# Performance work log

Hardware: AMD Instinct MI355X
Metric: run time of the kernel (lower is better)

Reference implementation:

```python
import jax, jax.numpy as jnp
import numpy as np

D_MODEL = 1024
N_HEADS = 16
N_KV = 4
HD = D_MODEL // N_HEADS  # 64
N_REP = N_HEADS // N_KV
WINDOW = 128
SCALE = HD ** -0.5
B, T = 2, 2048


def _rope(x):
    # x: [B, H, T, hd]; half-split rotate_half RoPE, base 10000
    t = x.shape[2]
    hd = x.shape[-1]
    inv_freq = 1.0 / (10000.0 ** (jnp.arange(0, hd, 2, dtype=jnp.float32) / hd))
    freqs = jnp.arange(t, dtype=jnp.float32)[:, None] * inv_freq[None, :]  # [T, hd/2]
    cos = jnp.cos(freqs)[None, None]  # [1,1,T,hd/2]
    sin = jnp.sin(freqs)[None, None]
    x1, x2 = x[..., : hd // 2], x[..., hd // 2:]
    return jnp.concatenate([x1 * cos - x2 * sin, x1 * sin + x2 * cos], axis=-1)


def setup_inputs() -> dict:
    key = jax.random.key(0)
    ks = jax.random.split(key, 6)
    s = 0.02
    return {
        "query": jax.random.normal(ks[0], (B, T, D_MODEL), dtype=jnp.float32),
        "Wq": jax.random.normal(ks[1], (D_MODEL, D_MODEL), dtype=jnp.float32) * s,
        "Wk": jax.random.normal(ks[2], (N_KV * HD, D_MODEL), dtype=jnp.float32) * s,
        "Wv": jax.random.normal(ks[3], (N_KV * HD, D_MODEL), dtype=jnp.float32) * s,
        "W1": jax.random.normal(ks[4], (4 * D_MODEL, D_MODEL), dtype=jnp.float32) * s,
        "W2": jax.random.normal(ks[5], (D_MODEL, 4 * D_MODEL), dtype=jnp.float32) * s,
    }


def reference(query, Wq, Wk, Wv, W1, W2):
    b, t, _ = query.shape
    # QKV projections (nn.Linear, no bias): x @ W.T
    q = (query @ Wq.T).reshape(b, t, N_HEADS, HD).transpose(0, 2, 1, 3)  # [B,H,T,hd]
    k = (query @ Wk.T).reshape(b, t, N_KV, HD).transpose(0, 2, 1, 3)    # [B,Hkv,T,hd]
    v = (query @ Wv.T).reshape(b, t, N_KV, HD).transpose(0, 2, 1, 3)
    # Rotary embeddings on q/k (self-attention)
    q = _rope(q)
    k = _rope(k)
    # GQA: repeat kv heads (kv-head-major ordering, matches torch expand+reshape)
    k = jnp.repeat(k, N_REP, axis=1)
    v = jnp.repeat(v, N_REP, axis=1)
    # scores + causal sliding-window band mask (True = masked)
    scores = jnp.einsum("bhqd,bhkd->bhqk", q, k) * SCALE
    i = jnp.arange(t)[:, None]
    j = jnp.arange(t)[None, :]
    mask = (j > i) | (j < i - (WINDOW - 1))  # causal window of size WINDOW
    scores = jnp.where(mask[None, None], jnp.float32(-1e30), scores)
    attn = jax.nn.softmax(scores, axis=-1)
    out = jnp.einsum("bhqk,bhkd->bhqd", attn, v)
    out = out.transpose(0, 2, 1, 3).reshape(b, t, D_MODEL)
    # out_proj: Linear(d,4d) -> SiLU -> Linear(4d,d)
    h = out @ W1.T
    h = h * jax.nn.sigmoid(h)
    return h @ W2.T
```

## Files before the change

kernel.cpp:

```cpp
#include <hip/hip_runtime.h>
#include <math.h>


typedef __bf16 bf16x8 __attribute__((ext_vector_type(8)));
typedef __bf16 bf16x4 __attribute__((ext_vector_type(4)));
typedef float  f32x4  __attribute__((ext_vector_type(4)));

extern __shared__ __align__(16) char smem[];

#define GLOAD_LDS16(g, l) __builtin_amdgcn_global_load_lds(               \
    (const __attribute__((address_space(1))) void*)(g),                   \
    (__attribute__((address_space(3))) void*)(l), 16, 0, 0)

__device__ __forceinline__ unsigned pk2(float a, float b) {
    union { __bf16 h[2]; unsigned u; } t;
    t.h[0] = (__bf16)a; t.h[1] = (__bf16)b;
    return t.u;
}

__device__ __forceinline__ int xcd_swz(int bid, int n) {
    return (bid & 7) * (n >> 3) + (bid >> 3);
}

__global__ __launch_bounds__(256) void MultiAttention_60722247631706_conv(
    const float* x, const float* Wq, const float* Wk, const float* Wv,
    const float* W1, const float* W2, float* out, float* ws, int phase)
{
    __bf16* xbf    = (__bf16*)(ws + 6291456);
    __bf16* wqkvbf = (__bf16*)(ws + 8388608);
    __bf16* w1bf   = (__bf16*)(ws + 10485760);
    __bf16* w2bf   = (__bf16*)(ws + 8388608);
    const int tid = threadIdx.x;

    if (phase == 5) {
        const long long total4 = 9961472 / 4;
        for (long long i4 = (long long)blockIdx.x * 256 + tid; i4 < total4;
             i4 += (long long)gridDim.x * 256) {
            const long long i = i4 * 4;
            const float* src; __bf16* dst;
            if (i < 4194304)      { src = x  + i;             dst = xbf    + i; }
            else if (i < 5242880) { src = Wq + (i - 4194304); dst = wqkvbf + (i - 4194304); }
            else if (i < 5505024) { src = Wk + (i - 5242880); dst = wqkvbf + (i - 4194304); }
            else if (i < 5767168) { src = Wv + (i - 5505024); dst = wqkvbf + (i - 4194304); }
            else                  { src = W1 + (i - 5767168); dst = w1bf   + (i - 5767168); }
            const f32x4 v = *(const f32x4*)src;
            bf16x4 o;
            o[0] = (__bf16)v[0]; o[1] = (__bf16)v[1];
            o[2] = (__bf16)v[2]; o[3] = (__bf16)v[3];
            *(bf16x4*)dst = o;
        }
    } else {
        const long long total4 = 4194304 / 4;
        for (long long i4 = (long long)blockIdx.x * 256 + tid; i4 < total4;
             i4 += (long long)gridDim.x * 256) {
            const long long i = i4 * 4;
            const f32x4 v = *(const f32x4*)(W2 + i);
            bf16x4 o;
            o[0] = (__bf16)v[0]; o[1] = (__bf16)v[1];
            o[2] = (__bf16)v[2]; o[3] = (__bf16)v[3];
            *(bf16x4*)(w2bf + i) = o;
        }
        const f32x4 z = {0.f, 0.f, 0.f, 0.f};
        for (long long i4 = (long long)blockIdx.x * 256 + tid; i4 < total4;
             i4 += (long long)gridDim.x * 256) {
            *(f32x4*)(out + i4 * 4) = z;
        }
    }
}

__global__ __launch_bounds__(256, 4) void MultiAttention_60722247631706_attn(
    float* ws)
{
    const __bf16* qbf  = (const __bf16*)ws;
    const __bf16* kbf  = (const __bf16*)(ws + 2097152);
    const __bf16* vtbf = (const __bf16*)(ws + 2621440);
    __bf16*       obf  = (__bf16*)(ws + 8388608);

    const int sb  = xcd_swz(blockIdx.x, 1024);
    const int qt  = sb & 127;
    const int kvh = (sb >> 7) & 3;
    const int b   = sb >> 9;
    const int q0  = qt * 16;
    const int wb  = q0 - 128;

    const int tid  = threadIdx.x;
    const int w    = tid >> 6;
    const int lane = tid & 63;
    const int l16  = lane & 15;
    const int quad = lane >> 4;
    const int h    = kvh * 4 + w;

    const __bf16* Kb = kbf + (size_t)b * 2048 * 256 + kvh * 64;
    const __bf16* Vb = vtbf + (size_t)(b * 4 + kvh) * 64 * 2048;

    bf16x8 qf[2];
#pragma unroll
    for (int kk = 0; kk < 2; ++kk)
        qf[kk] = *(const bf16x8*)(qbf + (size_t)(b * 2048 + q0 + l16) * 1024
                                  + h * 64 + kk * 32 + quad * 8);

    f32x4 oacc[4];
#pragma unroll
    for (int dn = 0; dn < 4; ++dn) {
        f32x4 z = {0.f, 0.f, 0.f, 0.f};
        oacc[dn] = z;
    }
    float m_run = -1e30f, l_run = 0.f;
    const int kclip = -wb;

    for (int kb = 0; kb < 3; ++kb) {
        f32x4 s[4];
#pragma unroll
        for (int km = 0; km < 4; ++km) {
            f32x4 z = {0.f, 0.f, 0.f, 0.f};
            s[km] = z;
        }
#pragma unroll
        for (int kk = 0; kk < 2; ++kk) {
            bf16x8 kf[4];
#pragma unroll
            for (int km = 0; km < 4; ++km) {
                int row = wb + kb * 64 + km * 16 + l16;
                row = (row >= 0 && row < 2048) ? row : 0;
                kf[km] = *(const bf16x8*)(Kb + (size_t)row * 256
                                          + kk * 32 + quad * 8);
            }
#pragma unroll
            for (int km = 0; km < 4; ++km)
                s[km] = __builtin_amdgcn_mfma_f32_16x16x32_bf16(
                    kf[km], qf[kk], s[km], 0, 0, 0);
        }

        float mx = -1e30f;
#pragma unroll
        for (int km = 0; km < 4; ++km)
#pragma unroll
            for (int r = 0; r < 4; ++r) {
                const int kl  = kb * 64 + km * 16 + quad * 4 + r;
                const int dlt = kl - l16;
                const bool ok = (dlt >= 1) && (dlt <= 128) && (kl >= kclip);
                const float sv = ok ? s[km][r] : -1e30f;
                s[km][r] = sv;
                mx = fmaxf(mx, sv);
            }
        mx = fmaxf(mx, __shfl_xor(mx, 16));
        mx = fmaxf(mx, __shfl_xor(mx, 32));
        const float mnew = fmaxf(fmaxf(m_run, mx), -1e20f);
        const float corr = expf(m_run - mnew);
        m_run = mnew;
        float rowsum = 0.f;
        unsigned cu[4][2];
#pragma unroll
        for (int km = 0; km < 4; ++km) {
#pragma unroll
            for (int r = 0; r < 4; ++r) {
                const float p = expf(s[km][r] - mnew);
                s[km][r] = p;
                rowsum += p;
            }
            cu[km][0] = pk2(s[km][0], s[km][1]);
            cu[km][1] = pk2(s[km][2], s[km][3]);
        }
        rowsum += __shfl_xor(rowsum, 16);
        rowsum += __shfl_xor(rowsum, 32);
        l_run = l_run * corr + rowsum;

#pragma unroll
        for (int r = 0; r < 4; ++r) {
            const float f = __shfl(corr, (lane & 48) | (quad * 4 + r));
            oacc[0][r] *= f; oacc[1][r] *= f;
            oacc[2][r] *= f; oacc[3][r] *= f;
        }

#pragma unroll
        for (int kk = 0; kk < 2; ++kk) {
            bf16x8 vf[4];
#pragma unroll
            for (int dn = 0; dn < 4; ++dn) {
                int t = wb + kb * 64 + kk * 32 + quad * 8;
                t = (t >= 0 && t <= 2040) ? t : 0;
                vf[dn] = *(const bf16x8*)(Vb + (size_t)(dn * 16 + l16) * 2048 + t);
            }
            const int srcA = ((quad & 1) * 32) + l16;
            const int hi   = quad >> 1;
            const unsigned a0 = (unsigned)__shfl((int)cu[2*kk  ][0], srcA);
            const unsigned a1 = (unsigned)__shfl((int)cu[2*kk  ][1], srcA);
            const unsigned b0 = (unsigned)__shfl((int)cu[2*kk+1][0], srcA);
            const unsigned b1 = (unsigned)__shfl((int)cu[2*kk+1][1], srcA);
            const unsigned c0 = (unsigned)__shfl((int)cu[2*kk  ][0], srcA + 16);
            const unsigned c1 = (unsigned)__shfl((int)cu[2*kk  ][1], srcA + 16);
            const unsigned d0 = (unsigned)__shfl((int)cu[2*kk+1][0], srcA + 16);
            const unsigned d1 = (unsigned)__shfl((int)cu[2*kk+1][1], srcA + 16);
            union { unsigned u[4]; bf16x8 v; } af;
            af.u[0] = hi ? b0 : a0;
            af.u[1] = hi ? b1 : a1;
            af.u[2] = hi ? d0 : c0;
            af.u[3] = hi ? d1 : c1;
#pragma unroll
            for (int dn = 0; dn < 4; ++dn)
                oacc[dn] = __builtin_amdgcn_mfma_f32_16x16x32_bf16(
                    af.v, vf[dn], oacc[dn], 0, 0, 0);
        }
    }

    const float rl = 1.f / l_run;
#pragma unroll
    for (int r = 0; r < 4; ++r) {
        const float f = __shfl(rl, (lane & 48) | (quad * 4 + r));
        const int q = q0 + quad * 4 + r;
        __bf16* op = obf + ((size_t)(b * 2048 + q)) * 1024 + h * 64 + l16;
#pragma unroll
        for (int dn = 0; dn < 4; ++dn)
            op[dn * 16] = (__bf16)(oacc[dn][r] * f);
    }
}

__global__ __launch_bounds__(256, 4) void MultiAttention_60722247631706_p0(
    float* ws)
{
    __bf16* qbf    = (__bf16*)ws;
    __bf16* kbf    = (__bf16*)(ws + 2097152);
    __bf16* vtbf   = (__bf16*)(ws + 2621440);
    __bf16* xbf    = (__bf16*)(ws + 6291456);
    __bf16* wqkvbf = (__bf16*)(ws + 8388608);

    const int tid = threadIdx.x;

    __bf16* As = (__bf16*)smem;
    __bf16* Bs = As + 64 * 64;

    const int bid  = xcd_swz(blockIdx.x, 768);
    const int tm   = bid / 12;
    const int tn   = bid % 12;
    const int w    = tid >> 6;
    const int lane = tid & 63;
    const int wr   = w >> 1;
    const int wc   = w & 1;
    const int l16  = lane & 15;
    const int quad = lane >> 4;
    const int srow = lane >> 3;
    const int sch  = ((lane & 7) ^ srow) * 8;

    const __bf16* ga0 = xbf    + (size_t)(tm * 64  + w * 16 + srow) * 1024 + sch;
    const __bf16* gb0 = wqkvbf + (size_t)(tn * 128 + w * 32 + srow) * 1024 + sch;

    f32x4 zero = {0.f, 0.f, 0.f, 0.f};
    f32x4 acc[2][4];
#pragma unroll
    for (int mi = 0; mi < 2; ++mi)
#pragma unroll
        for (int ni = 0; ni < 4; ++ni) acc[mi][ni] = zero;

    for (int k0 = 0; k0 < 1024; k0 += 64) {
#pragma unroll
        for (int i = 0; i < 2; ++i)
            GLOAD_LDS16(ga0 + (size_t)i * 8 * 1024 + k0, As + (w * 16 + i * 8) * 64);
#pragma unroll
        for (int i = 0; i < 4; ++i)
            GLOAD_LDS16(gb0 + (size_t)i * 8 * 1024 + k0, Bs + (w * 32 + i * 8) * 64);
        __syncthreads();
#pragma unroll
        for (int kk = 0; kk < 2; ++kk) {
            const int cs = ((kk * 4 + quad) ^ (l16 & 7)) * 8;
            bf16x8 af[2], bfr[4];
#pragma unroll
            for (int mi = 0; mi < 2; ++mi)
                af[mi] = *(const bf16x8*)(As + (size_t)(wr * 32 + mi * 16 + l16) * 64 + cs);
#pragma unroll
            for (int ni = 0; ni < 4; ++ni)
                bfr[ni] = *(const bf16x8*)(Bs + (size_t)(wc * 64 + ni * 16 + l16) * 64 + cs);
#pragma unroll
            for (int mi = 0; mi < 2; ++mi)
#pragma unroll
                for (int ni = 0; ni < 4; ++ni)
                    acc[mi][ni] = __builtin_amdgcn_mfma_f32_16x16x32_bf16(
                        af[mi], bfr[ni], acc[mi][ni], 0, 0, 0);
        }
        __syncthreads();
    }

    const int mbase = tm * 64 + wr * 32;
    const int nbase = tn * 128 + wc * 64;

    if (nbase < 1280) {
        const bool isQ = nbase < 1024;
        const float inv1 = powf(10000.f, -(float)l16 / 32.f);
        const float inv2 = powf(10000.f, -(float)(16 + l16) / 32.f);
#pragma unroll
        for (int mi = 0; mi < 2; ++mi) {
#pragma unroll
            for (int r = 0; r < 4; ++r) {
                const int m = mbase + mi * 16 + quad * 4 + r;
                const int t = m & 2047;
                float v0 = acc[mi][0][r], v1 = acc[mi][1][r];
                float v2 = acc[mi][2][r], v3 = acc[mi][3][r];
                const float a1 = (float)t * inv1, a2 = (float)t * inv2;
                const float c1 = cosf(a1), s1 = sinf(a1);
                const float c2 = cosf(a2), s2 = sinf(a2);
                float n0 = v0 * c1 - v2 * s1;
                float n2 = v0 * s1 + v2 * c1;
                float n1 = v1 * c2 - v3 * s2;
                float n3 = v1 * s2 + v3 * c2;
                if (isQ) { n0 *= 0.125f; n1 *= 0.125f; n2 *= 0.125f; n3 *= 0.125f; }
                __bf16* dst = isQ
                    ? qbf + (size_t)m * 1024 + nbase + l16
                    : kbf + (size_t)m * 256 + (nbase - 1024) + l16;
                dst[0]  = (__bf16)n0; dst[16] = (__bf16)n1;
                dst[32] = (__bf16)n2; dst[48] = (__bf16)n3;
            }
        }
    } else {
        const int kvh = (nbase - 1280) >> 6;
        const int bb  = mbase >> 11;
        const int tb  = mbase & 2047;
#pragma unroll
        for (int mi = 0; mi < 2; ++mi) {
#pragma unroll
            for (int ni = 0; ni < 4; ++ni) {
                const int d = ni * 16 + l16;
                bf16x4 pv;
                pv[0] = (__bf16)acc[mi][ni][0]; pv[1] = (__bf16)acc[mi][ni][1];
                pv[2] = (__bf16)acc[mi][ni][2]; pv[3] = (__bf16)acc[mi][ni][3];
                *(bf16x4*)(vtbf + ((size_t)(bb * 4 + kvh) * 64 + d) * 2048
                           + tb + mi * 16 + quad * 4) = pv;
            }
        }
    }
}

__global__ __launch_bounds__(256, 4) void MultiAttention_60722247631706_ffn1(
    float* ws)
{
    __bf16* obf  = (__bf16*)(ws + 8388608);
    __bf16* w1bf = (__bf16*)(ws + 10485760);
    __bf16* hbf  = (__bf16*)ws;

    const int tid = threadIdx.x;

    __bf16* As = (__bf16*)smem;
    __bf16* Bs = As + 128 * 64;

    const int bid  = xcd_swz(blockIdx.x, 1024);
    const int tm   = bid >> 5;
    const int tn   = bid & 31;
    const int w    = tid >> 6;
    const int lane = tid & 63;
    const int wr   = w >> 1;
    const int wc   = w & 1;
    const int l16  = lane & 15;
    const int quad = lane >> 4;
    const int srow = lane >> 3;
    const int sch  = ((lane & 7) ^ srow) * 8;

    const __bf16* ga0 = obf  + (size_t)(tm * 128 + w * 32 + srow) * 1024 + sch;
    const __bf16* gb0 = w1bf + (size_t)(tn * 128 + w * 32 + srow) * 1024 + sch;

    f32x4 zero = {0.f, 0.f, 0.f, 0.f};
    f32x4 acc[4][4];
#pragma unroll
    for (int mi = 0; mi < 4; ++mi)
#pragma unroll
        for (int ni = 0; ni < 4; ++ni) acc[mi][ni] = zero;

    for (int k0 = 0; k0 < 1024; k0 += 64) {
#pragma unroll
        for (int i = 0; i < 4; ++i) {
            GLOAD_LDS16(ga0 + (size_t)i * 8 * 1024 + k0, As + (w * 32 + i * 8) * 64);
            GLOAD_LDS16(gb0 + (size_t)i * 8 * 1024 + k0, Bs + (w * 32 + i * 8) * 64);
        }
        __syncthreads();
#pragma unroll
        for (int kk = 0; kk < 2; ++kk) {
            const int cs = ((kk * 4 + quad) ^ (l16 & 7)) * 8;
            bf16x8 af[4], bfr[4];
#pragma unroll
            for (int mi = 0; mi < 4; ++mi)
                af[mi] = *(const bf16x8*)(As + (size_t)(wr * 64 + mi * 16 + l16) * 64 + cs);
#pragma unroll
            for (int ni = 0; ni < 4; ++ni)
                bfr[ni] = *(const bf16x8*)(Bs + (size_t)(wc * 64 + ni * 16 + l16) * 64 + cs);
#pragma unroll
            for (int mi = 0; mi < 4; ++mi)
#pragma unroll
                for (int ni = 0; ni < 4; ++ni)
                    acc[mi][ni] = __builtin_amdgcn_mfma_f32_16x16x32_bf16(
                        af[mi], bfr[ni], acc[mi][ni], 0, 0, 0);
        }
        __syncthreads();
    }

#pragma unroll
    for (int mi = 0; mi < 4; ++mi) {
#pragma unroll
        for (int r = 0; r < 4; ++r) {
            const int m = tm * 128 + wr * 64 + mi * 16 + quad * 4 + r;
            __bf16* hp = hbf + (size_t)m * 4096 + tn * 128 + wc * 64 + l16;
#pragma unroll
            for (int ni = 0; ni < 4; ++ni) {
                const float v = acc[mi][ni][r];
                hp[ni * 16] = (__bf16)(v / (1.f + expf(-v)));
            }
        }
    }
}

__global__ __launch_bounds__(256, 4) void MultiAttention_60722247631706_ffn2(
    float* out, float* ws)
{
    __bf16* hbf  = (__bf16*)ws;
    __bf16* w2bf = (__bf16*)(ws + 8388608);

    int bid = xcd_swz(blockIdx.x, 1024);
    const int ks = bid >> 9;  bid &= 511;
    const int tm = bid >> 3;
    const int tn = bid & 7;
    const int kbase = ks * 2048;

    const int tid  = threadIdx.x;
    const int w    = tid >> 6;
    const int lane = tid & 63;
    const int wr   = w >> 1;
    const int wc   = w & 1;
    const int l16  = lane & 15;
    const int quad = lane >> 4;
    const int srow = lane >> 3;
    const int sch  = ((lane & 7) ^ srow) * 8;

    __bf16* As = (__bf16*)smem;
    __bf16* Bs = As + 64 * 64;

    const __bf16* ga0 = hbf  + (size_t)(tm * 64  + w * 16 + srow) * 4096 + kbase + sch;
    const __bf16* gb0 = w2bf + (size_t)(tn * 128 + w * 32 + srow) * 4096 + kbase + sch;

    f32x4 zero = {0.f, 0.f, 0.f, 0.f};
    f32x4 acc[2][4];
#pragma unroll
    for (int mi = 0; mi < 2; ++mi)
#pragma unroll
        for (int ni = 0; ni < 4; ++ni) acc[mi][ni] = zero;

    for (int k0 = 0; k0 < 2048; k0 += 64) {
#pragma unroll
        for (int i = 0; i < 2; ++i)
            GLOAD_LDS16(ga0 + (size_t)i * 8 * 4096 + k0, As + (w * 16 + i * 8) * 64);
#pragma unroll
        for (int i = 0; i < 4; ++i)
            GLOAD_LDS16(gb0 + (size_t)i * 8 * 4096 + k0, Bs + (w * 32 + i * 8) * 64);
        __syncthreads();
#pragma unroll
        for (int kk = 0; kk < 2; ++kk) {
            const int cs = ((kk * 4 + quad) ^ (l16 & 7)) * 8;
            bf16x8 af[2], bfr[4];
#pragma unroll
            for (int mi = 0; mi < 2; ++mi)
                af[mi] = *(const bf16x8*)(As + (size_t)(wr * 32 + mi * 16 + l16) * 64 + cs);
#pragma unroll
            for (int ni = 0; ni < 4; ++ni)
                bfr[ni] = *(const bf16x8*)(Bs + (size_t)(wc * 64 + ni * 16 + l16) * 64 + cs);
#pragma unroll
            for (int mi = 0; mi < 2; ++mi)
#pragma unroll
                for (int ni = 0; ni < 4; ++ni)
                    acc[mi][ni] = __builtin_amdgcn_mfma_f32_16x16x32_bf16(
                        af[mi], bfr[ni], acc[mi][ni], 0, 0, 0);
        }
        __syncthreads();
    }

#pragma unroll
    for (int mi = 0; mi < 2; ++mi) {
#pragma unroll
        for (int r = 0; r < 4; ++r) {
            const int m = tm * 64 + wr * 32 + mi * 16 + quad * 4 + r;
            float* op = out + (size_t)m * 1024 + tn * 128 + wc * 64 + l16;
#pragma unroll
            for (int ni = 0; ni < 4; ++ni)
                atomicAdd(op + ni * 16, acc[mi][ni][r]);
        }
    }
}

extern "C" void kernel_launch(void* const* d_in, const int* in_sizes, int n_in,
                              void* d_out, int out_size, void* d_ws, size_t ws_size,
                              hipStream_t stream)
{
    const float* x  = (const float*)d_in[0];
    const float* Wq = (const float*)d_in[1];
    const float* Wk = (const float*)d_in[2];
    const float* Wv = (const float*)d_in[3];
    const float* W1 = (const float*)d_in[4];
    const float* W2 = (const float*)d_in[5];
    float* out = (float*)d_out;
    float* ws  = (float*)d_ws;

    const int P0_LDS   = (64 + 128) * 64 * 2;
    const int FFN1_LDS = 2 * 128 * 64 * 2;
    const int FFN2_LDS = (64 + 128) * 64 * 2;

    MultiAttention_60722247631706_conv<<<2048, 256, 0, stream>>>(
        x, Wq, Wk, Wv, W1, W2, out, ws, 5);
    MultiAttention_60722247631706_p0<<<768, 256, P0_LDS, stream>>>(ws);
    MultiAttention_60722247631706_attn<<<1024, 256, 0, stream>>>(ws);
    MultiAttention_60722247631706_ffn1<<<1024, 256, FFN1_LDS, stream>>>(ws);
    MultiAttention_60722247631706_conv<<<1024, 256, 0, stream>>>(
        x, Wq, Wk, Wv, W1, W2, out, ws, 6);
    MultiAttention_60722247631706_ffn2<<<1024, 256, FFN2_LDS, stream>>>(out, ws);
}
```

Baseline: 247.0 us.

## Pre-tile bf16 operands into MFMA fragment order and drop LDS staging in GEMMs

The conversion kernels now write x, Wqkv, W1 and W2 in a 16x32 fragment-tiled layout. The attention and FFN1 epilogues write their outputs in that same tiled layout. The three GEMMs then load MFMA operands straight from global memory as contiguous 16-byte vectors, with no LDS staging and no __syncthreads. FFN2 also moves to a 128x128 tile with 512 blocks. This removes LDS traffic and barriers, but every wave now reloads the same operands from L2 with no shared reuse inside a block, and global latency is not hidden by any prefetch.

Measured after the change: 344.5 us. 1.39x slower.

```diff
diff --git a/kernel.cpp b/kernel.cpp
--- a/kernel.cpp
+++ b/kernel.cpp
@@ -5,12 +5,6 @@
 typedef __bf16 bf16x8 __attribute__((ext_vector_type(8)));
 typedef __bf16 bf16x4 __attribute__((ext_vector_type(4)));
 typedef float  f32x4  __attribute__((ext_vector_type(4)));
-
-extern __shared__ __align__(16) char smem[];
-
-#define GLOAD_LDS16(g, l) __builtin_amdgcn_global_load_lds(               \
-    (const __attribute__((address_space(1))) void*)(g),                   \
-    (__attribute__((address_space(3))) void*)(l), 16, 0, 0)
 
 __device__ __forceinline__ unsigned pk2(float a, float b) {
     union { __bf16 h[2]; unsigned u; } t;
@@ -22,49 +16,72 @@
     return (bid & 7) * (n >> 3) + (bid >> 3);
 }
 
-__global__ __launch_bounds__(256) void MultiAttention_60722247631706_conv(
+__device__ __forceinline__ void fm_chunk(const float* src, __bf16* dst8) {
+    const f32x4 a = *(const f32x4*)src;
+    const f32x4 b = *(const f32x4*)(src + 4);
+    bf16x8 o;
+    o[0] = (__bf16)a[0]; o[1] = (__bf16)a[1];
+    o[2] = (__bf16)a[2]; o[3] = (__bf16)a[3];
+    o[4] = (__bf16)b[0]; o[5] = (__bf16)b[1];
+    o[6] = (__bf16)b[2]; o[7] = (__bf16)b[3];
+    *(bf16x8*)dst8 = o;
+}
+
+__global__ __launch_bounds__(256) void MultiAttention_60722247631706_conv5(
     const float* x, const float* Wq, const float* Wk, const float* Wv,
-    const float* W1, const float* W2, float* out, float* ws, int phase)
-{
-    __bf16* xbf    = (__bf16*)(ws + 6291456);
-    __bf16* wqkvbf = (__bf16*)(ws + 8388608);
-    __bf16* w1bf   = (__bf16*)(ws + 10485760);
-    __bf16* w2bf   = (__bf16*)(ws + 8388608);
+    const float* W1, float* out, float* ws)
+{
+    __bf16* xt    = (__bf16*)(ws + 6291456);
+    __bf16* wqkvt = (__bf16*)(ws + 8388608);
+    __bf16* w1t   = (__bf16*)(ws + 10485760);
     const int tid = threadIdx.x;
 
-    if (phase == 5) {
-        const long long total4 = 9961472 / 4;
-        for (long long i4 = (long long)blockIdx.x * 256 + tid; i4 < total4;
-             i4 += (long long)gridDim.x * 256) {
-            const long long i = i4 * 4;
-            const float* src; __bf16* dst;
-            if (i < 4194304)      { src = x  + i;             dst = xbf    + i; }
-            else if (i < 5242880) { src = Wq + (i - 4194304); dst = wqkvbf + (i - 4194304); }
-            else if (i < 5505024) { src = Wk + (i - 5242880); dst = wqkvbf + (i - 4194304); }
-            else if (i < 5767168) { src = Wv + (i - 5505024); dst = wqkvbf + (i - 4194304); }
-            else                  { src = W1 + (i - 5767168); dst = w1bf   + (i - 5767168); }
-            const f32x4 v = *(const f32x4*)src;
-            bf16x4 o;
-            o[0] = (__bf16)v[0]; o[1] = (__bf16)v[1];
-            o[2] = (__bf16)v[2]; o[3] = (__bf16)v[3];
-            *(bf16x4*)dst = o;
-        }
-    } else {
-        const long long total4 = 4194304 / 4;
-        for (long long i4 = (long long)blockIdx.x * 256 + tid; i4 < total4;
-             i4 += (long long)gridDim.x * 256) {
-            const long long i = i4 * 4;
-            const f32x4 v = *(const f32x4*)(W2 + i);
-            bf16x4 o;
-            o[0] = (__bf16)v[0]; o[1] = (__bf16)v[1];
-            o[2] = (__bf16)v[2]; o[3] = (__bf16)v[3];
-            *(bf16x4*)(w2bf + i) = o;
-        }
-        const f32x4 z = {0.f, 0.f, 0.f, 0.f};
-        for (long long i4 = (long long)blockIdx.x * 256 + tid; i4 < total4;
-             i4 += (long long)gridDim.x * 256) {
-            *(f32x4*)(out + i4 * 4) = z;
-        }
+    const int XC = 524288, WQC = 196608, W1C = 524288;
+    const int total = XC + WQC + W1C;
+    for (int i = blockIdx.x * 256 + tid; i < total;
+         i += gridDim.x * 256) {
+        int c; const float* srcm; __bf16* dstm; int ldsrc = 1024;
+        int rowoff = 0;
+        if (i < XC)            { c = i;            srcm = x;  dstm = xt; }
+        else if (i < XC + WQC) { c = i - XC;       srcm = 0;  dstm = wqkvt; }
+        else                   { c = i - XC - WQC; srcm = W1; dstm = w1t; }
+        const int kq  = c & 3;
+        const int nin = (c >> 2) & 15;
+        const int kt  = (c >> 6) & 31;
+        const int nt  = c >> 11;
+        const int row = nt * 16 + nin;
+        const int col = kt * 32 + kq * 8;
+        const float* src;
+        if (srcm) {
+            src = srcm + (size_t)row * ldsrc + col;
+        } else {
+            if (row < 1024)      src = Wq + (size_t)row * 1024 + col;
+            else if (row < 1280) src = Wk + (size_t)(row - 1024) * 1024 + col;
+            else                 src = Wv + (size_t)(row - 1280) * 1024 + col;
+        }
+        fm_chunk(src, dstm + (size_t)c * 8);
+        (void)rowoff;
+    }
+    const f32x4 z = {0.f, 0.f, 0.f, 0.f};
+    for (int i4 = blockIdx.x * 256 + tid; i4 < 1048576;
+         i4 += gridDim.x * 256) {
+        *(f32x4*)(out + (size_t)i4 * 4) = z;
+    }
+}
+
+__global__ __launch_bounds__(256) void MultiAttention_60722247631706_conv6(
+    const float* W2, float* ws)
+{
+    __bf16* w2t = (__bf16*)(ws + 8388608);
+    const int tid = threadIdx.x;
+    for (int c = blockIdx.x * 256 + tid; c < 524288;
+         c += gridDim.x * 256) {
+        const int kq  = c & 3;
+        const int nin = (c >> 2) & 15;
+        const int kt  = (c >> 6) & 127;
+        const int nt  = c >> 13;
+        const float* src = W2 + (size_t)(nt * 16 + nin) * 4096 + kt * 32 + kq * 8;
+        fm_chunk(src, w2t + (size_t)c * 8);
     }
 }
 
@@ -204,14 +221,14 @@
     }
 
     const float rl = 1.f / l_run;
+    __bf16* ob = obf + ((size_t)(b * 128 + qt) * 32 + h * 2) * 512 + l16;
 #pragma unroll
     for (int r = 0; r < 4; ++r) {
         const float f = __shfl(rl, (lane & 48) | (quad * 4 + r));
-        const int q = q0 + quad * 4 + r;
-        __bf16* op = obf + ((size_t)(b * 2048 + q)) * 1024 + h * 64 + l16;
+        __bf16* obr = ob + (quad * 4 + r) * 32;
 #pragma unroll
         for (int dn = 0; dn < 4; ++dn)
-            op[dn * 16] = (__bf16)(oacc[dn][r] * f);
+            obr[(dn >> 1) * 512 + (dn & 1) * 16] = (__bf16)(oacc[dn][r] * f);
     }
 }
 
@@ -221,14 +238,10 @@
     __bf16* qbf    = (__bf16*)ws;
     __bf16* kbf    = (__bf16*)(ws + 2097152);
     __bf16* vtbf   = (__bf16*)(ws + 2621440);
-    __bf16* xbf    = (__bf16*)(ws + 6291456);
-    __bf16* wqkvbf = (__bf16*)(ws + 8388608);
-
-    const int tid = threadIdx.x;
-
-    __bf16* As = (__bf16*)smem;
-    __bf16* Bs = As + 64 * 64;
-
+    const __bf16* xt    = (const __bf16*)(ws + 6291456);
+    const __bf16* wqkvt = (const __bf16*)(ws + 8388608);
+
+    const int tid  = threadIdx.x;
     const int bid  = xcd_swz(blockIdx.x, 768);
     const int tm   = bid / 12;
     const int tn   = bid % 12;
@@ -238,11 +251,7 @@
     const int wc   = w & 1;
     const int l16  = lane & 15;
     const int quad = lane >> 4;
-    const int srow = lane >> 3;
-    const int sch  = ((lane & 7) ^ srow) * 8;
-
-    const __bf16* ga0 = xbf    + (size_t)(tm * 64  + w * 16 + srow) * 1024 + sch;
-    const __bf16* gb0 = wqkvbf + (size_t)(tn * 128 + w * 32 + srow) * 1024 + sch;
+    const int lo   = l16 * 32 + quad * 8;
 
     f32x4 zero = {0.f, 0.f, 0.f, 0.f};
     f32x4 acc[2][4];
@@ -253,22 +262,17 @@
 
     for (int k0 = 0; k0 < 1024; k0 += 64) {
 #pragma unroll
-        for (int i = 0; i < 2; ++i)
-            GLOAD_LDS16(ga0 + (size_t)i * 8 * 1024 + k0, As + (w * 16 + i * 8) * 64);
-#pragma unroll
-        for (int i = 0; i < 4; ++i)
-            GLOAD_LDS16(gb0 + (size_t)i * 8 * 1024 + k0, Bs + (w * 32 + i * 8) * 64);
-        __syncthreads();
-#pragma unroll
         for (int kk = 0; kk < 2; ++kk) {
-            const int cs = ((kk * 4 + quad) ^ (l16 & 7)) * 8;
+            const int kt = (k0 >> 5) + kk;
             bf16x8 af[2], bfr[4];
 #pragma unroll
             for (int mi = 0; mi < 2; ++mi)
-                af[mi] = *(const bf16x8*)(As + (size_t)(wr * 32 + mi * 16 + l16) * 64 + cs);
+                af[mi] = *(const bf16x8*)(xt +
+                    ((size_t)(tm * 4 + wr * 2 + mi) * 32 + kt) * 512 + lo);
 #pragma unroll
             for (int ni = 0; ni < 4; ++ni)
-                bfr[ni] = *(const bf16x8*)(Bs + (size_t)(wc * 64 + ni * 16 + l16) * 64 + cs);
+                bfr[ni] = *(const bf16x8*)(wqkvt +
+                    ((size_t)(tn * 8 + wc * 4 + ni) * 32 + kt) * 512 + lo);
 #pragma unroll
             for (int mi = 0; mi < 2; ++mi)
 #pragma unroll
@@ -276,7 +280,6 @@
                     acc[mi][ni] = __builtin_amdgcn_mfma_f32_16x16x32_bf16(
                         af[mi], bfr[ni], acc[mi][ni], 0, 0, 0);
         }
-        __syncthreads();
     }
 
     const int mbase = tm * 64 + wr * 32;
@@ -331,15 +334,11 @@
 __global__ __launch_bounds__(256, 4) void MultiAttention_60722247631706_ffn1(
     float* ws)
 {
-    __bf16* obf  = (__bf16*)(ws + 8388608);
-    __bf16* w1bf = (__bf16*)(ws + 10485760);
-    __bf16* hbf  = (__bf16*)ws;
-
-    const int tid = threadIdx.x;
-
-    __bf16* As = (__bf16*)smem;
-    __bf16* Bs = As + 128 * 64;
-
+    const __bf16* ot  = (const __bf16*)(ws + 8388608);
+    const __bf16* w1t = (const __bf16*)(ws + 10485760);
+    __bf16*       ht  = (__bf16*)ws;
+
+    const int tid  = threadIdx.x;
     const int bid  = xcd_swz(blockIdx.x, 1024);
     const int tm   = bid >> 5;
     const int tn   = bid & 31;
@@ -349,11 +348,7 @@
     const int wc   = w & 1;
     const int l16  = lane & 15;
     const int quad = lane >> 4;
-    const int srow = lane >> 3;
-    const int sch  = ((lane & 7) ^ srow) * 8;
-
-    const __bf16* ga0 = obf  + (size_t)(tm * 128 + w * 32 + srow) * 1024 + sch;
-    const __bf16* gb0 = w1bf + (size_t)(tn * 128 + w * 32 + srow) * 1024 + sch;
+    const int lo   = l16 * 32 + quad * 8;
 
     f32x4 zero = {0.f, 0.f, 0.f, 0.f};
     f32x4 acc[4][4];
@@ -364,21 +359,17 @@
 
     for (int k0 = 0; k0 < 1024; k0 += 64) {
 #pragma unroll
-        for (int i = 0; i < 4; ++i) {
-            GLOAD_LDS16(ga0 + (size_t)i * 8 * 1024 + k0, As + (w * 32 + i * 8) * 64);
-            GLOAD_LDS16(gb0 + (size_t)i * 8 * 1024 + k0, Bs + (w * 32 + i * 8) * 64);
-        }
-        __syncthreads();
-#pragma unroll
         for (int kk = 0; kk < 2; ++kk) {
-            const int cs = ((kk * 4 + quad) ^ (l16 & 7)) * 8;
+            const int kt = (k0 >> 5) + kk;
             bf16x8 af[4], bfr[4];
 #pragma unroll
             for (int mi = 0; mi < 4; ++mi)
-                af[mi] = *(const bf16x8*)(As + (size_t)(wr * 64 + mi * 16 + l16) * 64 + cs);
+                af[mi] = *(const bf16x8*)(ot +
+                    ((size_t)(tm * 8 + wr * 4 + mi) * 32 + kt) * 512 + lo);
 #pragma unroll
             for (int ni = 0; ni < 4; ++ni)
-                bfr[ni] = *(const bf16x8*)(Bs + (size_t)(wc * 64 + ni * 16 + l16) * 64 + cs);
+                bfr[ni] = *(const bf16x8*)(w1t +
+                    ((size_t)(tn * 8 + wc * 4 + ni) * 32 + kt) * 512 + lo);
 #pragma unroll
             for (int mi = 0; mi < 4; ++mi)
 #pragma unroll
@@ -386,19 +377,20 @@
                     acc[mi][ni] = __builtin_amdgcn_mfma_f32_16x16x32_bf16(
                         af[mi], bfr[ni], acc[mi][ni], 0, 0, 0);
         }
-        __syncthreads();
     }
 
 #pragma unroll
     for (int mi = 0; mi < 4; ++mi) {
+        const int mtile = tm * 8 + wr * 4 + mi;
+        __bf16* hb = ht + ((size_t)mtile * 128 + (tn * 4 + wc * 2)) * 512 + l16;
 #pragma unroll
         for (int r = 0; r < 4; ++r) {
-            const int m = tm * 128 + wr * 64 + mi * 16 + quad * 4 + r;
-            __bf16* hp = hbf + (size_t)m * 4096 + tn * 128 + wc * 64 + l16;
+            __bf16* hr = hb + (quad * 4 + r) * 32;
 #pragma unroll
             for (int ni = 0; ni < 4; ++ni) {
                 const float v = acc[mi][ni][r];
-                hp[ni * 16] = (__bf16)(v / (1.f + expf(-v)));
+                hr[(ni >> 1) * 512 + (ni & 1) * 16] =
+                    (__bf16)(v / (1.f + expf(-v)));
             }
         }
     }
@@ -407,14 +399,14 @@
 __global__ __launch_bounds__(256, 4) void MultiAttention_60722247631706_ffn2(
     float* out, float* ws)
 {
-    __bf16* hbf  = (__bf16*)ws;
-    __bf16* w2bf = (__bf16*)(ws + 8388608);
-
-    int bid = xcd_swz(blockIdx.x, 1024);
-    const int ks = bid >> 9;  bid &= 511;
+    const __bf16* ht  = (const __bf16*)ws;
+    const __bf16* w2t = (const __bf16*)(ws + 8388608);
+
+    int bid = xcd_swz(blockIdx.x, 512);
+    const int ks = bid >> 8;  bid &= 255;
     const int tm = bid >> 3;
     const int tn = bid & 7;
-    const int kbase = ks * 2048;
+    const int ktb = ks * 64;
 
     const int tid  = threadIdx.x;
     const int w    = tid >> 6;
@@ -423,55 +415,42 @@
     const int wc   = w & 1;
     const int l16  = lane & 15;
     const int quad = lane >> 4;
-    const int srow = lane >> 3;
-    const int sch  = ((lane & 7) ^ srow) * 8;
-
-    __bf16* As = (__bf16*)smem;
-    __bf16* Bs = As + 64 * 64;
-
-    const __bf16* ga0 = hbf  + (size_t)(tm * 64  + w * 16 + srow) * 4096 + kbase + sch;
-    const __bf16* gb0 = w2bf + (size_t)(tn * 128 + w * 32 + srow) * 4096 + kbase + sch;
+    const int lo   = l16 * 32 + quad * 8;
 
     f32x4 zero = {0.f, 0.f, 0.f, 0.f};
-    f32x4 acc[2][4];
-#pragma unroll
-    for (int mi = 0; mi < 2; ++mi)
+    f32x4 acc[4][4];
+#pragma unroll
+    for (int mi = 0; mi < 4; ++mi)
 #pragma unroll
         for (int ni = 0; ni < 4; ++ni) acc[mi][ni] = zero;
 
     for (int k0 = 0; k0 < 2048; k0 += 64) {
 #pragma unroll
-        for (int i = 0; i < 2; ++i)
-            GLOAD_LDS16(ga0 + (size_t)i * 8 * 4096 + k0, As + (w * 16 + i * 8) * 64);
-#pragma unroll
-        for (int i = 0; i < 4; ++i)
-            GLOAD_LDS16(gb0 + (size_t)i * 8 * 4096 + k0, Bs + (w * 32 + i * 8) * 64);
-        __syncthreads();
-#pragma unroll
         for (int kk = 0; kk < 2; ++kk) {
-            const int cs = ((kk * 4 + quad) ^ (l16 & 7)) * 8;
-            bf16x8 af[2], bfr[4];
-#pragma unroll
-            for (int mi = 0; mi < 2; ++mi)
-                af[mi] = *(const bf16x8*)(As + (size_t)(wr * 32 + mi * 16 + l16) * 64 + cs);
+            const int kt = ktb + (k0 >> 5) + kk;
+            bf16x8 af[4], bfr[4];
+#pragma unroll
+            for (int mi = 0; mi < 4; ++mi)
+                af[mi] = *(const bf16x8*)(ht +
+                    ((size_t)(tm * 8 + wr * 4 + mi) * 128 + kt) * 512 + lo);
 #pragma unroll
             for (int ni = 0; ni < 4; ++ni)
-                bfr[ni] = *(const bf16x8*)(Bs + (size_t)(wc * 64 + ni * 16 + l16) * 64 + cs);
-#pragma unroll
-            for (int mi = 0; mi < 2; ++mi)
+                bfr[ni] = *(const bf16x8*)(w2t +
+                    ((size_t)(tn * 8 + wc * 4 + ni) * 128 + kt) * 512 + lo);
+#pragma unroll
+            for (int mi = 0; mi < 4; ++mi)
 #pragma unroll
                 for (int ni = 0; ni < 4; ++ni)
                     acc[mi][ni] = __builtin_amdgcn_mfma_f32_16x16x32_bf16(
                         af[mi], bfr[ni], acc[mi][ni], 0, 0, 0);
         }
-        __syncthreads();
-    }
-
-#pragma unroll
-    for (int mi = 0; mi < 2; ++mi) {
+    }
+
+#pragma unroll
+    for (int mi = 0; mi < 4; ++mi) {
 #pragma unroll
         for (int r = 0; r < 4; ++r) {
-            const int m = tm * 64 + wr * 32 + mi * 16 + quad * 4 + r;
+            const int m = tm * 128 + wr * 64 + mi * 16 + quad * 4 + r;
             float* op = out + (size_t)m * 1024 + tn * 128 + wc * 64 + l16;
 #pragma unroll
             for (int ni = 0; ni < 4; ++ni)
@@ -493,16 +472,11 @@
     float* out = (float*)d_out;
     float* ws  = (float*)d_ws;
 
-    const int P0_LDS   = (64 + 128) * 64 * 2;
-    const int FFN1_LDS = 2 * 128 * 64 * 2;
-    const int FFN2_LDS = (64 + 128) * 64 * 2;
-
-    MultiAttention_60722247631706_conv<<<2048, 256, 0, stream>>>(
-        x, Wq, Wk, Wv, W1, W2, out, ws, 5);
-    MultiAttention_60722247631706_p0<<<768, 256, P0_LDS, stream>>>(ws);
+    MultiAttention_60722247631706_conv5<<<2048, 256, 0, stream>>>(
+        x, Wq, Wk, Wv, W1, out, ws);
+    MultiAttention_60722247631706_p0<<<768, 256, 0, stream>>>(ws);
     MultiAttention_60722247631706_attn<<<1024, 256, 0, stream>>>(ws);
-    MultiAttention_60722247631706_ffn1<<<1024, 256, FFN1_LDS, stream>>>(ws);
-    MultiAttention_60722247631706_conv<<<1024, 256, 0, stream>>>(
-        x, Wq, Wk, Wv, W1, W2, out, ws, 6);
-    MultiAttention_60722247631706_ffn2<<<1024, 256, FFN2_LDS, stream>>>(out, ws);
-}
+    MultiAttention_60722247631706_ffn1<<<1024, 256, 0, stream>>>(ws);
+    MultiAttention_60722247631706_conv6<<<1024, 256, 0, stream>>>(W2, ws);
+    MultiAttention_60722247631706_ffn2<<<512, 256, 0, stream>>>(out, ws);
+}
```

## Pre-swizzle FFN weights into MFMA fragment order and load B directly from global

Applied to the files above, without the earlier changes.

The fp32-to-bf16 conversion of W1 and W2 now writes them in a tiled layout that matches the MFMA B-fragment order. The FFN GEMMs can then read B operands straight from global memory into registers, with no LDS staging. This shrinks LDS use per block and removes LDS traffic and bank conflicts for B. The cost is that B-operand reuse across waves now depends on L1/L2 caching instead of shared memory, and global-load latency is exposed inside the k-loop. The zeroing of the output is also moved into the first conversion kernel.

Measured after the change: 282.9 us. +14.5%, slower.

```diff
diff --git a/kernel.cpp b/kernel.cpp
--- a/kernel.cpp
+++ b/kernel.cpp
@@ -22,49 +22,66 @@
     return (bid & 7) * (n >> 3) + (bid >> 3);
 }
 
-__global__ __launch_bounds__(256) void MultiAttention_60722247631706_conv(
+__device__ __forceinline__ void fm_chunk(const float* src, __bf16* dst8) {
+    const f32x4 a = *(const f32x4*)src;
+    const f32x4 b = *(const f32x4*)(src + 4);
+    bf16x8 o;
+    o[0] = (__bf16)a[0]; o[1] = (__bf16)a[1];
+    o[2] = (__bf16)a[2]; o[3] = (__bf16)a[3];
+    o[4] = (__bf16)b[0]; o[5] = (__bf16)b[1];
+    o[6] = (__bf16)b[2]; o[7] = (__bf16)b[3];
+    *(bf16x8*)dst8 = o;
+}
+
+__global__ __launch_bounds__(256) void MultiAttention_60722247631706_conv5(
     const float* x, const float* Wq, const float* Wk, const float* Wv,
-    const float* W1, const float* W2, float* out, float* ws, int phase)
+    const float* W1, float* out, float* ws)
 {
     __bf16* xbf    = (__bf16*)(ws + 6291456);
     __bf16* wqkvbf = (__bf16*)(ws + 8388608);
-    __bf16* w1bf   = (__bf16*)(ws + 10485760);
-    __bf16* w2bf   = (__bf16*)(ws + 8388608);
+    __bf16* w1t    = (__bf16*)(ws + 10485760);
     const int tid = threadIdx.x;
 
-    if (phase == 5) {
-        const long long total4 = 9961472 / 4;
-        for (long long i4 = (long long)blockIdx.x * 256 + tid; i4 < total4;
-             i4 += (long long)gridDim.x * 256) {
-            const long long i = i4 * 4;
-            const float* src; __bf16* dst;
-            if (i < 4194304)      { src = x  + i;             dst = xbf    + i; }
-            else if (i < 5242880) { src = Wq + (i - 4194304); dst = wqkvbf + (i - 4194304); }
-            else if (i < 5505024) { src = Wk + (i - 5242880); dst = wqkvbf + (i - 4194304); }
-            else if (i < 5767168) { src = Wv + (i - 5505024); dst = wqkvbf + (i - 4194304); }
-            else                  { src = W1 + (i - 5767168); dst = w1bf   + (i - 5767168); }
-            const f32x4 v = *(const f32x4*)src;
-            bf16x4 o;
-            o[0] = (__bf16)v[0]; o[1] = (__bf16)v[1];
-            o[2] = (__bf16)v[2]; o[3] = (__bf16)v[3];
-            *(bf16x4*)dst = o;
-        }
-    } else {
-        const long long total4 = 4194304 / 4;
-        for (long long i4 = (long long)blockIdx.x * 256 + tid; i4 < total4;
-             i4 += (long long)gridDim.x * 256) {
-            const long long i = i4 * 4;
-            const f32x4 v = *(const f32x4*)(W2 + i);
-            bf16x4 o;
-            o[0] = (__bf16)v[0]; o[1] = (__bf16)v[1];
-            o[2] = (__bf16)v[2]; o[3] = (__bf16)v[3];
-            *(bf16x4*)(w2bf + i) = o;
-        }
-        const f32x4 z = {0.f, 0.f, 0.f, 0.f};
-        for (long long i4 = (long long)blockIdx.x * 256 + tid; i4 < total4;
-             i4 += (long long)gridDim.x * 256) {
-            *(f32x4*)(out + i4 * 4) = z;
-        }
+    const long long total4 = 5767168 / 4;
+    for (long long i4 = (long long)blockIdx.x * 256 + tid; i4 < total4;
+         i4 += (long long)gridDim.x * 256) {
+        const long long i = i4 * 4;
+        const float* src; __bf16* dst;
+        if (i < 4194304)      { src = x  + i;             dst = xbf    + i; }
+        else if (i < 5242880) { src = Wq + (i - 4194304); dst = wqkvbf + (i - 4194304); }
+        else if (i < 5505024) { src = Wk + (i - 5242880); dst = wqkvbf + (i - 4194304); }
+        else                  { src = Wv + (i - 5505024); dst = wqkvbf + (i - 4194304); }
+        const f32x4 v = *(const f32x4*)src;
+        bf16x4 o;
+        o[0] = (__bf16)v[0]; o[1] = (__bf16)v[1];
+        o[2] = (__bf16)v[2]; o[3] = (__bf16)v[3];
+        *(bf16x4*)dst = o;
+    }
+    for (int c = blockIdx.x * 256 + tid; c < 524288; c += gridDim.x * 256) {
+        const int kq  = c & 3;
+        const int nin = (c >> 2) & 15;
+        const int kt  = (c >> 6) & 31;
+        const int nt  = c >> 11;
+        const float* src = W1 + (size_t)(nt * 16 + nin) * 1024 + kt * 32 + kq * 8;
+        fm_chunk(src, w1t + (size_t)c * 8);
+    }
+    const f32x4 z = {0.f, 0.f, 0.f, 0.f};
+    for (int i4 = blockIdx.x * 256 + tid; i4 < 1048576; i4 += gridDim.x * 256)
+        *(f32x4*)(out + (size_t)i4 * 4) = z;
+}
+
+__global__ __launch_bounds__(256) void MultiAttention_60722247631706_conv6(
+    const float* W2, float* ws)
+{
+    __bf16* w2t = (__bf16*)(ws + 8388608);
+    const int tid = threadIdx.x;
+    for (int c = blockIdx.x * 256 + tid; c < 524288; c += gridDim.x * 256) {
+        const int kq  = c & 3;
+        const int nin = (c >> 2) & 15;
+        const int kt  = (c >> 6) & 127;
+        const int nt  = c >> 13;
+        const float* src = W2 + (size_t)(nt * 16 + nin) * 4096 + kt * 32 + kq * 8;
+        fm_chunk(src, w2t + (size_t)c * 8);
     }
 }
 
@@ -331,14 +348,13 @@
 __global__ __launch_bounds__(256, 4) void MultiAttention_60722247631706_ffn1(
     float* ws)
 {
-    __bf16* obf  = (__bf16*)(ws + 8388608);
-    __bf16* w1bf = (__bf16*)(ws + 10485760);
-    __bf16* hbf  = (__bf16*)ws;
+    __bf16*       obf = (__bf16*)(ws + 8388608);
+    const __bf16* w1t = (const __bf16*)(ws + 10485760);
+    __bf16*       hbf = (__bf16*)ws;
 
     const int tid = threadIdx.x;
 
     __bf16* As = (__bf16*)smem;
-    __bf16* Bs = As + 128 * 64;
 
     const int bid  = xcd_swz(blockIdx.x, 1024);
     const int tm   = bid >> 5;
@@ -351,9 +367,10 @@
     const int quad = lane >> 4;
     const int srow = lane >> 3;
     const int sch  = ((lane & 7) ^ srow) * 8;
-
-    const __bf16* ga0 = obf  + (size_t)(tm * 128 + w * 32 + srow) * 1024 + sch;
-    const __bf16* gb0 = w1bf + (size_t)(tn * 128 + w * 32 + srow) * 1024 + sch;
+    const int lo   = l16 * 32 + quad * 8;
+
+    const __bf16* ga0 = obf + (size_t)(tm * 128 + w * 32 + srow) * 1024 + sch;
+    const __bf16* wb0 = w1t + (size_t)(tn * 8 + wc * 4) * 32 * 512 + lo;
 
     f32x4 zero = {0.f, 0.f, 0.f, 0.f};
     f32x4 acc[4][4];
@@ -364,21 +381,21 @@
 
     for (int k0 = 0; k0 < 1024; k0 += 64) {
 #pragma unroll
-        for (int i = 0; i < 4; ++i) {
+        for (int i = 0; i < 4; ++i)
             GLOAD_LDS16(ga0 + (size_t)i * 8 * 1024 + k0, As + (w * 32 + i * 8) * 64);
-            GLOAD_LDS16(gb0 + (size_t)i * 8 * 1024 + k0, Bs + (w * 32 + i * 8) * 64);
-        }
         __syncthreads();
 #pragma unroll
         for (int kk = 0; kk < 2; ++kk) {
+            const int kt = (k0 >> 5) + kk;
+            bf16x8 bfr[4];
+#pragma unroll
+            for (int ni = 0; ni < 4; ++ni)
+                bfr[ni] = *(const bf16x8*)(wb0 + ((size_t)ni * 32 + kt) * 512);
             const int cs = ((kk * 4 + quad) ^ (l16 & 7)) * 8;
-            bf16x8 af[4], bfr[4];
+            bf16x8 af[4];
 #pragma unroll
             for (int mi = 0; mi < 4; ++mi)
                 af[mi] = *(const bf16x8*)(As + (size_t)(wr * 64 + mi * 16 + l16) * 64 + cs);
-#pragma unroll
-            for (int ni = 0; ni < 4; ++ni)
-                bfr[ni] = *(const bf16x8*)(Bs + (size_t)(wc * 64 + ni * 16 + l16) * 64 + cs);
 #pragma unroll
             for (int mi = 0; mi < 4; ++mi)
 #pragma unroll
@@ -407,14 +424,15 @@
 __global__ __launch_bounds__(256, 4) void MultiAttention_60722247631706_ffn2(
     float* out, float* ws)
 {
-    __bf16* hbf  = (__bf16*)ws;
-    __bf16* w2bf = (__bf16*)(ws + 8388608);
+    const __bf16* hbf = (const __bf16*)ws;
+    const __bf16* w2t = (const __bf16*)(ws + 8388608);
 
     int bid = xcd_swz(blockIdx.x, 1024);
     const int ks = bid >> 9;  bid &= 511;
     const int tm = bid >> 3;
     const int tn = bid & 7;
     const int kbase = ks * 2048;
+    const int ktb   = ks * 64;
 
     const int tid  = threadIdx.x;
     const int w    = tid >> 6;
@@ -425,12 +443,12 @@
     const int quad = lane >> 4;
     const int srow = lane >> 3;
     const int sch  = ((lane & 7) ^ srow) * 8;
+    const int lo   = l16 * 32 + quad * 8;
 
     __bf16* As = (__bf16*)smem;
-    __bf16* Bs = As + 64 * 64;
-
-    const __bf16* ga0 = hbf  + (size_t)(tm * 64  + w * 16 + srow) * 4096 + kbase + sch;
-    const __bf16* gb0 = w2bf + (size_t)(tn * 128 + w * 32 + srow) * 4096 + kbase + sch;
+
+    const __bf16* ga0 = hbf + (size_t)(tm * 64 + w * 16 + srow) * 4096 + kbase + sch;
+    const __bf16* wb0 = w2t + (size_t)(tn * 8 + wc * 4) * 128 * 512 + lo;
 
     f32x4 zero = {0.f, 0.f, 0.f, 0.f};
     f32x4 acc[2][4];
@@ -443,20 +461,19 @@
 #pragma unroll
         for (int i = 0; i < 2; ++i)
             GLOAD_LDS16(ga0 + (size_t)i * 8 * 4096 + k0, As + (w * 16 + i * 8) * 64);
-#pragma unroll
-        for (int i = 0; i < 4; ++i)
-            GLOAD_LDS16(gb0 + (size_t)i * 8 * 4096 + k0, Bs + (w * 32 + i * 8) * 64);
         __syncthreads();
 #pragma unroll
         for (int kk = 0; kk < 2; ++kk) {
+            const int kt = ktb + (k0 >> 5) + kk;
+            bf16x8 bfr[4];
+#pragma unroll
+            for (int ni = 0; ni < 4; ++ni)
+                bfr[ni] = *(const bf16x8*)(wb0 + ((size_t)ni * 128 + kt) * 512);
             const int cs = ((kk * 4 + quad) ^ (l16 & 7)) * 8;
-            bf16x8 af[2], bfr[4];
+            bf16x8 af[2];
 #pragma unroll
             for (int mi = 0; mi < 2; ++mi)
                 af[mi] = *(const bf16x8*)(As + (size_t)(wr * 32 + mi * 16 + l16) * 64 + cs);
-#pragma unroll
-            for (int ni = 0; ni < 4; ++ni)
-                bfr[ni] = *(const bf16x8*)(Bs + (size_t)(wc * 64 + ni * 16 + l16) * 64 + cs);
 #pragma unroll
             for (int mi = 0; mi < 2; ++mi)
 #pragma unroll
@@ -494,15 +511,14 @@
     float* ws  = (float*)d_ws;
 
     const int P0_LDS   = (64 + 128) * 64 * 2;
-    const int FFN1_LDS = 2 * 128 * 64 * 2;
-    const int FFN2_LDS = (64 + 128) * 64 * 2;
-
-    MultiAttention_60722247631706_conv<<<2048, 256, 0, stream>>>(
-        x, Wq, Wk, Wv, W1, W2, out, ws, 5);
+    const int FFN1_LDS = 128 * 64 * 2;
+    const int FFN2_LDS = 64 * 64 * 2;
+
+    MultiAttention_60722247631706_conv5<<<2048, 256, 0, stream>>>(
+        x, Wq, Wk, Wv, W1, out, ws);
     MultiAttention_60722247631706_p0<<<768, 256, P0_LDS, stream>>>(ws);
     MultiAttention_60722247631706_attn<<<1024, 256, 0, stream>>>(ws);
     MultiAttention_60722247631706_ffn1<<<1024, 256, FFN1_LDS, stream>>>(ws);
-    MultiAttention_60722247631706_conv<<<1024, 256, 0, stream>>>(
-        x, Wq, Wk, Wv, W1, W2, out, ws, 6);
+    MultiAttention_60722247631706_conv6<<<1024, 256, 0, stream>>>(W2, ws);
     MultiAttention_60722247631706_ffn2<<<1024, 256, FFN2_LDS, stream>>>(out, ws);
 }
```
